# Performance work log

Hardware: AMD Instinct MI355X
Metric: run time of the kernel (lower is better)

The kernel has to match this reference:

```python
import jax, jax.numpy as jnp
import numpy as np

N = 128            # particles
NR = N * (N - 1)   # fully-connected directed edges = 16256
FPRIME = 32        # attention projection dim
F = 16             # input features per particle
B = 64             # batch


def _edge_indices(n):
    # Reproduce assign_matrices: itertools.product order, skip self-loops.
    r, s = np.meshgrid(np.arange(n), np.arange(n), indexing='ij')
    r, s = r.ravel(), s.ravel()
    keep = r != s
    return r[keep].astype(np.int32), s[keep].astype(np.int32)


def setup_inputs() -> dict:
    key = jax.random.key(0)
    k1, k2, k3 = jax.random.split(key, 3)
    x = jax.random.normal(k1, (B, F, N), dtype=jnp.float32)
    w = jax.random.normal(k2, (FPRIME, F), dtype=jnp.float32) * 0.05  # 'random_normal' init
    a = jax.random.normal(k3, (1, 2 * FPRIME), dtype=jnp.float32) * 0.05
    recv, send = _edge_indices(N)
    return {"x": x, "w": w, "a": a,
            "recv": jnp.asarray(recv), "send": jnp.asarray(send)}


def reference(x, w, a, recv, send):
    # wh[b,n,g] = sum_f x[b,f,n] * w[g,f]   (tf.tensordot(inputs, w, [1,1]))
    wh = jnp.einsum('bfn,gf->bng', x, w)            # (B, N, Fprime)
    # tensordot(wh, Rr/Rs) with one-hot Rr/Rs == gather by receiver/sender index
    whi = wh[:, recv, :]                            # (B, Nr, Fprime)
    whj = wh[:, send, :]                            # (B, Nr, Fprime)
    # a @ concat([whi, whj], feat axis) == a1 @ whi + a2 @ whj
    a1, a2 = a[0, :FPRIME], a[0, FPRIME:]
    out = whi @ a1 + whj @ a2                        # (B, Nr)
    return out[:, :, None]                           # (B, Nr, 1)
```

## Files before the change

### kernel.cpp

```cpp
#include <hip/hip_runtime.h>

#define BATCH 64
#define FDIM  16
#define NDIM  128
#define FP    32
#define NEDGE (NDIM * (NDIM - 1))
#define NEDGE4 (NEDGE / 4)

__global__ __launch_bounds__(256) void gat_edge_fused(
    const float* __restrict__ x,
    const float* __restrict__ w,
    const float* __restrict__ a,
    const int*   __restrict__ recv,
    const int*   __restrict__ send,
    float*       __restrict__ out)
{
    __shared__ float v1s[FDIM];
    __shared__ float v2s[FDIM];
    __shared__ float s1s[NDIM];
    __shared__ float s2s[NDIM];

    const int b = blockIdx.y;
    const int t = threadIdx.x;

    if (t < 2 * FDIM) {
        const int f = t & (FDIM - 1);
        const float* av = a + ((t < FDIM) ? 0 : FP);
        float acc = 0.f;
#pragma unroll
        for (int g = 0; g < FP; ++g)
            acc += av[g] * w[g * FDIM + f];
        if (t < FDIM) v1s[f] = acc;
        else          v2s[f] = acc;
    }
    __syncthreads();

    if (t < NDIM) {
        const float* xb = x + (size_t)b * FDIM * NDIM + t;
        float acc1 = 0.f, acc2 = 0.f;
#pragma unroll
        for (int f = 0; f < FDIM; ++f) {
            const float xv = xb[f * NDIM];
            acc1 += xv * v1s[f];
            acc2 += xv * v2s[f];
        }
        s1s[t] = acc1;
        s2s[t] = acc2;
    }
    __syncthreads();

    const int e4 = blockIdx.x * blockDim.x + t;
    if (e4 < NEDGE4) {
        const int4 r = ((const int4*)recv)[e4];
        const int4 s = ((const int4*)send)[e4];
        float4 o;
        o.x = s1s[r.x] + s2s[s.x];
        o.y = s1s[r.y] + s2s[s.y];
        o.z = s1s[r.z] + s2s[s.z];
        o.w = s1s[r.w] + s2s[s.w];
        ((float4*)(out + (size_t)b * NEDGE))[e4] = o;
    }
}

extern "C" void kernel_launch(void* const* d_in, const int* in_sizes, int n_in,
                              void* d_out, int out_size, void* d_ws, size_t ws_size,
                              hipStream_t stream) {
    const float* x    = (const float*)d_in[0];
    const float* w    = (const float*)d_in[1];
    const float* a    = (const float*)d_in[2];
    const int*   recv = (const int*)d_in[3];
    const int*   send = (const int*)d_in[4];
    float*       out  = (float*)d_out;

    dim3 grid((NEDGE4 + 255) / 256, BATCH);
    gat_edge_fused<<<grid, 256, 0, stream>>>(x, w, a, recv, send, out);
}
```

Baseline: 63.64 us.

## Prefetch x and edge indices before syncs, split all threads across s1/s2, use 8 chunks

The x loads and the recv/send index loads are issued at kernel start so they overlap the small w·a reduction and the barrier. The s1/s2 computation is split so threads 0-127 produce s1 and 128-255 produce s2, rather than 128 threads doing both. The grid shrinks from 16 to 8 edge chunks per batch, and each thread handles up to two float4 outputs, which halves the redundant per-block prologue work. Fewer blocks means less parallelism, and each thread holds more registers for the prefetched values.

```diff
diff --git a/kernel.cpp b/kernel.cpp
--- a/kernel.cpp
+++ b/kernel.cpp
@@ -6,6 +6,8 @@
 #define FP    32
 #define NEDGE (NDIM * (NDIM - 1))
 #define NEDGE4 (NEDGE / 4)
+#define CHUNKS 8
+#define E4PB  (NEDGE4 / CHUNKS)
 
 __global__ __launch_bounds__(256) void gat_edge_fused(
     const float* __restrict__ x,
@@ -22,43 +24,68 @@
 
     const int b = blockIdx.y;
     const int t = threadIdx.x;
+    const int n = t & (NDIM - 1);
+
+    const float* xb = x + (size_t)b * (FDIM * NDIM) + n;
+    float xv[FDIM];
+#pragma unroll
+    for (int f = 0; f < FDIM; ++f)
+        xv[f] = xb[f * NDIM];
+
+    const int e4_0 = blockIdx.x * E4PB + t;
+    const int e4_1 = e4_0 + 256;
+    const bool has1 = (t + 256) < E4PB;
+    const int4 r0 = ((const int4*)recv)[e4_0];
+    const int4 c0 = ((const int4*)send)[e4_0];
+    int4 r1 = r0, c1 = c0;
+    if (has1) {
+        r1 = ((const int4*)recv)[e4_1];
+        c1 = ((const int4*)send)[e4_1];
+    }
 
     if (t < 2 * FDIM) {
         const int f = t & (FDIM - 1);
         const float* av = a + ((t < FDIM) ? 0 : FP);
-        float acc = 0.f;
+        float p0 = 0.f, p1 = 0.f, p2 = 0.f, p3 = 0.f;
 #pragma unroll
-        for (int g = 0; g < FP; ++g)
-            acc += av[g] * w[g * FDIM + f];
+        for (int g = 0; g < FP; g += 4) {
+            p0 += av[g + 0] * w[(g + 0) * FDIM + f];
+            p1 += av[g + 1] * w[(g + 1) * FDIM + f];
+            p2 += av[g + 2] * w[(g + 2) * FDIM + f];
+            p3 += av[g + 3] * w[(g + 3) * FDIM + f];
+        }
+        const float acc = (p0 + p1) + (p2 + p3);
         if (t < FDIM) v1s[f] = acc;
         else          v2s[f] = acc;
     }
     __syncthreads();
 
-    if (t < NDIM) {
-        const float* xb = x + (size_t)b * FDIM * NDIM + t;
-        float acc1 = 0.f, acc2 = 0.f;
+    {
+        const float* vv = (t < NDIM) ? v1s : v2s;
+        float p0 = 0.f, p1 = 0.f;
 #pragma unroll
-        for (int f = 0; f < FDIM; ++f) {
-            const float xv = xb[f * NDIM];
-            acc1 += xv * v1s[f];
-            acc2 += xv * v2s[f];
+        for (int f = 0; f < FDIM; f += 2) {
+            p0 += xv[f]     * vv[f];
+            p1 += xv[f + 1] * vv[f + 1];
         }
-        s1s[t] = acc1;
-        s2s[t] = acc2;
+        if (t < NDIM) s1s[n] = p0 + p1;
+        else          s2s[n] = p0 + p1;
     }
     __syncthreads();
 
-    const int e4 = blockIdx.x * blockDim.x + t;
-    if (e4 < NEDGE4) {
-        const int4 r = ((const int4*)recv)[e4];
-        const int4 s = ((const int4*)send)[e4];
-        float4 o;
-        o.x = s1s[r.x] + s2s[s.x];
-        o.y = s1s[r.y] + s2s[s.y];
-        o.z = s1s[r.z] + s2s[s.z];
-        o.w = s1s[r.w] + s2s[s.w];
-        ((float4*)(out + (size_t)b * NEDGE))[e4] = o;
+    float4* ob = (float4*)(out + (size_t)b * NEDGE);
+    float4 o;
+    o.x = s1s[r0.x] + s2s[c0.x];
+    o.y = s1s[r0.y] + s2s[c0.y];
+    o.z = s1s[r0.z] + s2s[c0.z];
+    o.w = s1s[r0.w] + s2s[c0.w];
+    ob[e4_0] = o;
+    if (has1) {
+        o.x = s1s[r1.x] + s2s[c1.x];
+        o.y = s1s[r1.y] + s2s[c1.y];
+        o.z = s1s[r1.z] + s2s[c1.z];
+        o.w = s1s[r1.w] + s2s[c1.w];
+        ob[e4_1] = o;
     }
 }
 
@@ -72,6 +99,6 @@
     const int*   send = (const int*)d_in[4];
     float*       out  = (float*)d_out;
 
-    dim3 grid((NEDGE4 + 255) / 256, BATCH);
+    dim3 grid(CHUNKS, BATCH);
     gat_edge_fused<<<grid, 256, 0, stream>>>(x, w, a, recv, send, out);
 }
```

After: 64.03 us. Within noise of the previous version (+0.6%).
